# Kernel tuning notes

Hardware: AMD Instinct MI355X
Metric: run time of the kernel (lower is better)

The kernel has to match this reference:

```python
import jax, jax.numpy as jnp
import numpy as np

B, N, C = 2, 384, 128
D = C // 4          # bottleneck_dim
H = 128             # time_mlp_hidden_dim


def setup_inputs() -> dict:
    key = jax.random.key(0)
    ks = jax.random.split(key, 12)
    s = 0.02
    return {
        "edge_embed": jax.random.normal(ks[0], (B, N, N, C), jnp.float32),
        "edge_mask": jax.random.randint(ks[1], (B, N, N), 0, 2, jnp.int32),
        "r3_t": jax.random.uniform(ks[2], (B,), jnp.float32),
        # linear params stored as [in, out]
        "Wg": jax.random.normal(ks[3], (C, D), jnp.float32) * s,
        "bg": jnp.zeros((D,), jnp.float32),
        "Wv": jax.random.normal(ks[4], (C, D), jnp.float32) * s,
        "bv": jnp.zeros((D,), jnp.float32),
        "Wd": jax.random.normal(ks[5], (C, D), jnp.float32) * s,
        "bd": jnp.zeros((D,), jnp.float32),
        "Wo": jax.random.normal(ks[6], (D, C), jnp.float32) * s,
        "bo": jnp.zeros((C,), jnp.float32),
        "W1": jax.random.normal(ks[7], (1, H), jnp.float32) * s,
        "b1": jnp.zeros((H,), jnp.float32),
        "W2": jax.random.normal(ks[8], (H, 2 * C), jnp.float32) * s,
        "b2": jnp.zeros((2 * C,), jnp.float32),
    }


def reference(edge_embed, edge_mask, r3_t, Wg, bg, Wv, bv, Wd, bd, Wo, bo, W1, b1, W2, b2):
    Bb, Nn, _, Cc = edge_embed.shape
    P = edge_embed.reshape(Bb, Nn * Nn, Cc)          # [B, N^2, C]
    m = (edge_mask.reshape(Bb, Nn * Nn, 1) != 0)
    mf = m.astype(P.dtype)

    fP = P @ Wg + bg                                 # [B, N^2, D]
    gP = P @ Wv + bv                                 # [B, N^2, D]
    fP = jnp.where(m, fP, jnp.asarray(-1e8, P.dtype))
    w = jax.nn.softmax(fP, axis=1)                   # softmax over all edges
    w = w * mf
    w = w / (w.sum(axis=1, keepdims=True) + 1e-8)

    V = jnp.einsum('bnd,bne->bde', w, gP)            # [B, D, D] global context

    hP = jax.nn.softmax(P @ Wd + bd, axis=2)         # softmax over channels
    O = jnp.einsum('bnd,bde->bne', hP, V)            # redistribute
    O = (O @ Wo + bo).reshape(Bb, Nn, Nn, Cc)

    # FiLM conditioned on timestep (torch GELU is exact erf form)
    t = r3_t.reshape(Bb, 1)
    t_emb = jax.nn.gelu(t @ W1 + b1, approximate=False) @ W2 + b2
    scale, shift = jnp.split(t_emb, 2, axis=-1)
    O = O * (1 + scale[:, None, None, :]) + shift[:, None, None, :]

    return edge_embed + O
```

## Files before the change

### kernel.cpp

```cpp
#include <hip/hip_runtime.h>
#include <hip/hip_bf16.h>
#include <math.h>

#define N2 147456
#define CC 128
#define TILES 2304

#define WS_VACC 0
#define WS_S    2048
#define WS_FS   2112
#define WS_SH   2368

typedef __attribute__((ext_vector_type(8))) __bf16 bf16x8;
typedef __attribute__((ext_vector_type(4))) __bf16 bf16x4;
typedef __attribute__((ext_vector_type(4))) float f32x4;

#define MFMA16(a_, b_, c_) __builtin_amdgcn_mfma_f32_16x16x32_bf16((a_), (b_), (c_), 0, 0, 0)

__global__ __launch_bounds__(256) void k0_init(
    const float* __restrict__ r3t,
    const float* __restrict__ W1, const float* __restrict__ b1,
    const float* __restrict__ W2, const float* __restrict__ b2,
    float* __restrict__ ws)
{
    const int t = threadIdx.x, bx = blockIdx.x;
    if (bx > 0) {
        const int i = (bx - 1) * 256 + t;
        if (i < 2112) ws[i] = 0.0f;
        return;
    }
    __shared__ float h[2][128];
    {
        const int b = t >> 7, j = t & 127;
        const float x = r3t[b] * W1[j] + b1[j];
        h[b][j] = 0.5f * x * (1.0f + erff(x * 0.7071067811865475f));
    }
    __syncthreads();
    const int j2 = t;
    float acc0 = b2[j2], acc1 = b2[j2];
    for (int k = 0; k < 128; ++k) {
        const float w2 = W2[k * 256 + j2];
        acc0 += h[0][k] * w2;
        acc1 += h[1][k] * w2;
    }
    if (j2 < 128) {
        ws[WS_FS + j2]       = 1.0f + acc0;
        ws[WS_FS + 128 + j2] = 1.0f + acc1;
    } else {
        ws[WS_SH + (j2 - 128)]       = acc0;
        ws[WS_SH + 128 + (j2 - 128)] = acc1;
    }
}

__global__ __launch_bounds__(256, 3) void k1_accum(
    const float* __restrict__ P, const int* __restrict__ mask,
    const float* __restrict__ Wg, const float* __restrict__ bg,
    const float* __restrict__ Wv, const float* __restrict__ bv,
    float* __restrict__ ws)
{
    __shared__ __bf16 ef_t[32][72];
    __shared__ __bf16 gv_t[32][72];

    const int t  = threadIdx.x;
    const int b  = blockIdx.y;
    const int w  = t >> 6;
    const int l  = t & 63;
    const int lr = l & 15;
    const int lg = l >> 4;

    bf16x8 wfrag[2][2][4];
    #pragma unroll
    for (int nt = 0; nt < 2; ++nt)
      #pragma unroll
      for (int ks = 0; ks < 4; ++ks) {
        const int base = (ks * 32 + 8 * lg) * 32 + nt * 16 + lr;
        bf16x8 f0, f1;
        #pragma unroll
        for (int i = 0; i < 8; ++i) {
            f0[i] = (__bf16)Wg[base + i * 32];
            f1[i] = (__bf16)Wv[base + i * 32];
        }
        wfrag[0][nt][ks] = f0;
        wfrag[1][nt][ks] = f1;
      }
    const float bgv[2] = { bg[lr], bg[lr + 16] };
    const float bvv[2] = { bv[lr], bv[lr + 16] };

    const int mt = w >> 1, ntq = w & 1;
    f32x4 vacc = {0.f, 0.f, 0.f, 0.f};
    float accS = 0.f;
    const int sd = t >> 3, ss = t & 7;

    const float* Pb = P + (size_t)b * N2 * CC;
    const int*   mb = mask + (size_t)b * N2;

    for (int tile = blockIdx.x; tile < TILES; tile += gridDim.x) {
        const int row0 = tile * 64 + w * 16;
        const float* prow = Pb + (size_t)(row0 + lr) * CC + 8 * lg;

        bf16x8 afrag[4];
        #pragma unroll
        for (int ks = 0; ks < 4; ++ks) {
            const float4 a0 = *(const float4*)(prow + ks * 32);
            const float4 a1 = *(const float4*)(prow + ks * 32 + 4);
            bf16x8 f;
            f[0] = (__bf16)a0.x; f[1] = (__bf16)a0.y; f[2] = (__bf16)a0.z; f[3] = (__bf16)a0.w;
            f[4] = (__bf16)a1.x; f[5] = (__bf16)a1.y; f[6] = (__bf16)a1.z; f[7] = (__bf16)a1.w;
            afrag[ks] = f;
        }

        f32x4 facc0 = {0,0,0,0}, facc1 = {0,0,0,0}, gacc0 = {0,0,0,0}, gacc1 = {0,0,0,0};
        #pragma unroll
        for (int ks = 0; ks < 4; ++ks) {
            facc0 = MFMA16(afrag[ks], wfrag[0][0][ks], facc0);
            facc1 = MFMA16(afrag[ks], wfrag[0][1][ks], facc1);
            gacc0 = MFMA16(afrag[ks], wfrag[1][0][ks], gacc0);
            gacc1 = MFMA16(afrag[ks], wfrag[1][1][ks], gacc1);
        }

        const int4 mk4 = *(const int4*)&mb[row0 + lg * 4];
        const int mk[4] = { mk4.x, mk4.y, mk4.z, mk4.w };

        bf16x4 pe0, pe1, pg0, pg1;
        #pragma unroll
        for (int r = 0; r < 4; ++r) {
            pe0[r] = (__bf16)(mk[r] ? __expf(facc0[r] + bgv[0]) : 0.0f);
            pe1[r] = (__bf16)(mk[r] ? __expf(facc1[r] + bgv[1]) : 0.0f);
            pg0[r] = (__bf16)(gacc0[r] + bvv[0]);
            pg1[r] = (__bf16)(gacc1[r] + bvv[1]);
        }
        const int cbase = w * 16 + lg * 4;
        *(bf16x4*)&ef_t[lr     ][cbase] = pe0;
        *(bf16x4*)&ef_t[lr + 16][cbase] = pe1;
        *(bf16x4*)&gv_t[lr     ][cbase] = pg0;
        *(bf16x4*)&gv_t[lr + 16][cbase] = pg1;
        __syncthreads();

        #pragma unroll
        for (int ks = 0; ks < 2; ++ks) {
            const bf16x8 ea = *(const bf16x8*)&ef_t[mt  * 16 + lr][ks * 32 + 8 * lg];
            const bf16x8 gb = *(const bf16x8*)&gv_t[ntq * 16 + lr][ks * 32 + 8 * lg];
            vacc = MFMA16(ea, gb, vacc);
        }
        {
            const bf16x8 ev = *(const bf16x8*)&ef_t[sd][ss * 8];
            float s = 0.f;
            #pragma unroll
            for (int i = 0; i < 8; ++i) s += (float)ev[i];
            accS += s;
        }
        __syncthreads();
    }

    #pragma unroll
    for (int r = 0; r < 4; ++r) {
        const int d = mt * 16 + lg * 4 + r;
        const int e = ntq * 16 + lr;
        atomicAdd(ws + WS_VACC + b * 1024 + d * 32 + e, vacc[r]);
    }
    accS += __shfl_xor(accS, 1);
    accS += __shfl_xor(accS, 2);
    accS += __shfl_xor(accS, 4);
    if (ss == 0) atomicAdd(ws + WS_S + b * 32 + sd, accS);
}

__global__ __launch_bounds__(256, 3) void k3_out(
    const float* __restrict__ P,
    const float* __restrict__ Wd, const float* __restrict__ bd,
    const float* __restrict__ Wo, const float* __restrict__ bo,
    const float* __restrict__ ws, float* __restrict__ out)
{
    __shared__ float  u_lds[32][132];
    __shared__ __bf16 h_t[64][40];
    __shared__ float  fin_V[1024];
    __shared__ float  fin_fs[128];
    __shared__ float  fin_b2[128];

    const int t  = threadIdx.x;
    const int b  = blockIdx.y;
    const int w  = t >> 6, l = t & 63, lr = l & 15, lg = l >> 4;

    if (t < 128) {
        const float fs = ws[WS_FS + b * 128 + t];
        fin_fs[t] = fs;
        fin_b2[t] = bo[t] * fs + ws[WS_SH + b * 128 + t];
    }
    #pragma unroll
    for (int i = 0; i < 4; ++i) {
        const int idx = t + i * 256;
        const int d = idx >> 5;
        const float s = ws[WS_S + b * 32 + d];
        fin_V[idx] = ws[WS_VACC + b * 1024 + idx] / (s * (1.0f + 1e-8f));
    }

    bf16x8 wdfrag[2][4];
    #pragma unroll
    for (int nt = 0; nt < 2; ++nt)
      #pragma unroll
      for (int ks = 0; ks < 4; ++ks) {
        const int base = (ks * 32 + 8 * lg) * 32 + nt * 16 + lr;
        bf16x8 f;
        #pragma unroll
        for (int i = 0; i < 8; ++i) f[i] = (__bf16)Wd[base + i * 32];
        wdfrag[nt][ks] = f;
      }
    float bdv[8];
    #pragma unroll
    for (int r = 0; r < 4; ++r) {
        bdv[r]     = bd[lg * 4 + r];
        bdv[4 + r] = bd[16 + lg * 4 + r];
    }

    __syncthreads();

    #pragma unroll
    for (int i = 0; i < 16; ++i) {
        const int idx = t + i * 256;
        const int d = idx >> 7, c = idx & 127;
        float acc = 0.0f;
        #pragma unroll
        for (int e = 0; e < 32; ++e) acc += fin_V[d * 32 + e] * Wo[e * 128 + c];
        u_lds[d][c] = acc * fin_fs[c];
    }
    __syncthreads();

    bf16x8 ufrag[8];
    #pragma unroll
    for (int nt = 0; nt < 8; ++nt) {
        bf16x8 f;
        #pragma unroll
        for (int i = 0; i < 8; ++i) f[i] = (__bf16)u_lds[8 * lg + i][nt * 16 + lr];
        ufrag[nt] = f;
    }
    float b2v[8][4];
    #pragma unroll
    for (int nt = 0; nt < 8; ++nt) {
        const float4 v = *(const float4*)&fin_b2[nt * 16 + lg * 4];
        b2v[nt][0] = v.x; b2v[nt][1] = v.y; b2v[nt][2] = v.z; b2v[nt][3] = v.w;
    }

    const float* Pb = P + (size_t)b * N2 * CC;
    float*       Ob = out + (size_t)b * N2 * CC;

    for (int tile = TILES - 1 - blockIdx.x; tile >= 0; tile -= gridDim.x) {
        const int row0 = tile * 64 + w * 16;
        const float* prow = Pb + (size_t)(row0 + lr) * CC + 8 * lg;

        bf16x8 afrag[4];
        #pragma unroll
        for (int ks = 0; ks < 4; ++ks) {
            const float4 a0 = *(const float4*)(prow + ks * 32);
            const float4 a1 = *(const float4*)(prow + ks * 32 + 4);
            bf16x8 f;
            f[0] = (__bf16)a0.x; f[1] = (__bf16)a0.y; f[2] = (__bf16)a0.z; f[3] = (__bf16)a0.w;
            f[4] = (__bf16)a1.x; f[5] = (__bf16)a1.y; f[6] = (__bf16)a1.z; f[7] = (__bf16)a1.w;
            afrag[ks] = f;
        }

        f32x4 dacc0 = {0,0,0,0}, dacc1 = {0,0,0,0};
        #pragma unroll
        for (int ks = 0; ks < 4; ++ks) {
            dacc0 = MFMA16(wdfrag[0][ks], afrag[ks], dacc0);
            dacc1 = MFMA16(wdfrag[1][ks], afrag[ks], dacc1);
        }

        float v[8];
        #pragma unroll
        for (int r = 0; r < 4; ++r) {
            v[r]     = dacc0[r] + bdv[r];
            v[4 + r] = dacc1[r] + bdv[4 + r];
        }
        float m = v[0];
        #pragma unroll
        for (int j = 1; j < 8; ++j) m = fmaxf(m, v[j]);
        m = fmaxf(m, __shfl_xor(m, 16));
        m = fmaxf(m, __shfl_xor(m, 32));
        float e[8], s = 0.f;
        #pragma unroll
        for (int j = 0; j < 8; ++j) { e[j] = __expf(v[j] - m); s += e[j]; }
        s += __shfl_xor(s, 16);
        s += __shfl_xor(s, 32);
        const float inv = 1.0f / s;

        bf16x4 h0, h1;
        #pragma unroll
        for (int r = 0; r < 4; ++r) {
            h0[r] = (__bf16)(e[r] * inv);
            h1[r] = (__bf16)(e[4 + r] * inv);
        }
        const int hrow = w * 16 + lr;
        *(bf16x4*)&h_t[hrow][lg * 4]      = h0;
        *(bf16x4*)&h_t[hrow][16 + lg * 4] = h1;
        const bf16x8 hf = *(const bf16x8*)&h_t[hrow][8 * lg];

        #pragma unroll
        for (int nt = 0; nt < 8; ++nt) {
            f32x4 ci;
            ci[0] = b2v[nt][0]; ci[1] = b2v[nt][1]; ci[2] = b2v[nt][2]; ci[3] = b2v[nt][3];
            const f32x4 oacc = MFMA16(ufrag[nt], hf, ci);
            const size_t off = (size_t)(row0 + lr) * CC + nt * 16 + lg * 4;
            const float4 p4 = *(const float4*)(Pb + off);
            float4 o4;
            o4.x = p4.x + oacc[0]; o4.y = p4.y + oacc[1];
            o4.z = p4.z + oacc[2]; o4.w = p4.w + oacc[3];
            *(float4*)(Ob + off) = o4;
        }
    }
}

extern "C" void kernel_launch(void* const* d_in, const int* in_sizes, int n_in,
                              void* d_out, int out_size, void* d_ws, size_t ws_size,
                              hipStream_t stream) {
    const float* P   = (const float*)d_in[0];
    const int*   msk = (const int*)d_in[1];
    const float* r3t = (const float*)d_in[2];
    const float* Wg  = (const float*)d_in[3];
    const float* bg  = (const float*)d_in[4];
    const float* Wv  = (const float*)d_in[5];
    const float* bv  = (const float*)d_in[6];
    const float* Wd  = (const float*)d_in[7];
    const float* bd  = (const float*)d_in[8];
    const float* Wo  = (const float*)d_in[9];
    const float* bo  = (const float*)d_in[10];
    const float* W1  = (const float*)d_in[11];
    const float* b1  = (const float*)d_in[12];
    const float* W2  = (const float*)d_in[13];
    const float* b2  = (const float*)d_in[14];
    float* ws  = (float*)d_ws;
    float* out = (float*)d_out;

    hipLaunchKernelGGL(k0_init,  dim3(10),      dim3(256), 0, stream, r3t, W1, b1, W2, b2, ws);
    hipLaunchKernelGGL(k1_accum, dim3(384, 2),  dim3(256), 0, stream, P, msk, Wg, bg, Wv, bv, ws);
    hipLaunchKernelGGL(k3_out,   dim3(768, 2),  dim3(256), 0, stream, P, Wd, bd, Wo, bo, ws, out);
}
```

Before: 133.8 us.

## Hoist V·Wo prologue into a separate kernel and prefetch residual loads

The per-block prologue of the output kernel, which normalised V, multiplied it by Wo and repacked the result into bf16 MFMA fragments, moves into a new two-block mid kernel. That kernel writes the packed fragments and the fused bias/shift vector to the workspace. The output kernel now loads those fragments directly, drops its large LDS buffers, and raises its launch bound to 4 blocks per SM. The residual P loads for the epilogue are also issued at the start of each tile alongside the A-fragment loads, which adds register pressure, and the extra kernel launch adds a small serial cost.

```diff
diff --git a/kernel.cpp b/kernel.cpp
--- a/kernel.cpp
+++ b/kernel.cpp
@@ -6,10 +6,12 @@
 #define CC 128
 #define TILES 2304
 
-#define WS_VACC 0
-#define WS_S    2048
-#define WS_FS   2112
-#define WS_SH   2368
+#define WS_VACC  0
+#define WS_S     2048
+#define WS_FS    2112
+#define WS_SH    2368
+#define WS_UPACK 2624
+#define WS_B2P   6720
 
 typedef __attribute__((ext_vector_type(8))) __bf16 bf16x8;
 typedef __attribute__((ext_vector_type(4))) __bf16 bf16x4;
@@ -164,35 +166,73 @@
     if (ss == 0) atomicAdd(ws + WS_S + b * 32 + sd, accS);
 }
 
-__global__ __launch_bounds__(256, 3) void k3_out(
-    const float* __restrict__ P,
-    const float* __restrict__ Wd, const float* __restrict__ bd,
+__global__ __launch_bounds__(256) void k2_mid(
     const float* __restrict__ Wo, const float* __restrict__ bo,
-    const float* __restrict__ ws, float* __restrict__ out)
+    float* __restrict__ ws)
 {
-    __shared__ float  u_lds[32][132];
-    __shared__ __bf16 h_t[64][40];
-    __shared__ float  fin_V[1024];
-    __shared__ float  fin_fs[128];
-    __shared__ float  fin_b2[128];
-
-    const int t  = threadIdx.x;
-    const int b  = blockIdx.y;
-    const int w  = t >> 6, l = t & 63, lr = l & 15, lg = l >> 4;
-
-    if (t < 128) {
-        const float fs = ws[WS_FS + b * 128 + t];
-        fin_fs[t] = fs;
-        fin_b2[t] = bo[t] * fs + ws[WS_SH + b * 128 + t];
-    }
+    __shared__ float V[1024];
+    __shared__ float wo[32][128];
+    __shared__ float fs[128];
+    const int t = threadIdx.x, b = blockIdx.x;
+
+    if (t < 128) fs[t] = ws[WS_FS + b * 128 + t];
     #pragma unroll
     for (int i = 0; i < 4; ++i) {
         const int idx = t + i * 256;
         const int d = idx >> 5;
         const float s = ws[WS_S + b * 32 + d];
-        fin_V[idx] = ws[WS_VACC + b * 1024 + idx] / (s * (1.0f + 1e-8f));
-    }
-
+        V[idx] = ws[WS_VACC + b * 1024 + idx] / (s * (1.0f + 1e-8f));
+    }
+    #pragma unroll
+    for (int i = 0; i < 4; ++i) {
+        const int j = t + i * 256;
+        ((float4*)&wo[0][0])[j] = ((const float4*)Wo)[j];
+    }
+    __syncthreads();
+
+    const int c = t & 127, dh = t >> 7;
+    float wcol[32];
+    #pragma unroll
+    for (int e = 0; e < 32; ++e) wcol[e] = wo[e][c];
+    const float fsc = fs[c];
+    if (dh == 0) ws[WS_B2P + b * 128 + c] = bo[c] * fsc + ws[WS_SH + b * 128 + c];
+
+    __bf16* dst = (__bf16*)(ws + WS_UPACK);
+    #pragma unroll
+    for (int dd = 0; dd < 16; ++dd) {
+        const int d = dh * 16 + dd;
+        float acc = 0.0f;
+        #pragma unroll
+        for (int e = 0; e < 32; ++e) acc += V[d * 32 + e] * wcol[e];
+        acc *= fsc;
+        const int lg = d >> 3, ii = d & 7, nt = c >> 4, lr = c & 15;
+        dst[(((size_t)b * 8 + nt) * 64 + (lg * 16 + lr)) * 8 + ii] = (__bf16)acc;
+    }
+}
+
+__global__ __launch_bounds__(256, 4) void k3_out(
+    const float* __restrict__ P,
+    const float* __restrict__ Wd, const float* __restrict__ bd,
+    const float* __restrict__ ws, float* __restrict__ out)
+{
+    __shared__ __bf16 h_t[64][40];
+
+    const int t  = threadIdx.x;
+    const int b  = blockIdx.y;
+    const int w  = t >> 6, l = t & 63, lr = l & 15, lg = l >> 4;
+
+    bf16x8 ufrag[8];
+    {
+        const bf16x8* up = (const bf16x8*)(ws + WS_UPACK) + (size_t)b * 512 + l;
+        #pragma unroll
+        for (int nt = 0; nt < 8; ++nt) ufrag[nt] = up[nt * 64];
+    }
+    float b2v[8][4];
+    #pragma unroll
+    for (int nt = 0; nt < 8; ++nt) {
+        const float4 v = *(const float4*)(ws + WS_B2P + b * 128 + nt * 16 + lg * 4);
+        b2v[nt][0] = v.x; b2v[nt][1] = v.y; b2v[nt][2] = v.z; b2v[nt][3] = v.w;
+    }
     bf16x8 wdfrag[2][4];
     #pragma unroll
     for (int nt = 0; nt < 2; ++nt)
@@ -211,46 +251,29 @@
         bdv[4 + r] = bd[16 + lg * 4 + r];
     }
 
-    __syncthreads();
-
-    #pragma unroll
-    for (int i = 0; i < 16; ++i) {
-        const int idx = t + i * 256;
-        const int d = idx >> 7, c = idx & 127;
-        float acc = 0.0f;
-        #pragma unroll
-        for (int e = 0; e < 32; ++e) acc += fin_V[d * 32 + e] * Wo[e * 128 + c];
-        u_lds[d][c] = acc * fin_fs[c];
-    }
-    __syncthreads();
-
-    bf16x8 ufrag[8];
-    #pragma unroll
-    for (int nt = 0; nt < 8; ++nt) {
-        bf16x8 f;
-        #pragma unroll
-        for (int i = 0; i < 8; ++i) f[i] = (__bf16)u_lds[8 * lg + i][nt * 16 + lr];
-        ufrag[nt] = f;
-    }
-    float b2v[8][4];
-    #pragma unroll
-    for (int nt = 0; nt < 8; ++nt) {
-        const float4 v = *(const float4*)&fin_b2[nt * 16 + lg * 4];
-        b2v[nt][0] = v.x; b2v[nt][1] = v.y; b2v[nt][2] = v.z; b2v[nt][3] = v.w;
-    }
-
     const float* Pb = P + (size_t)b * N2 * CC;
     float*       Ob = out + (size_t)b * N2 * CC;
 
     for (int tile = TILES - 1 - blockIdx.x; tile >= 0; tile -= gridDim.x) {
         const int row0 = tile * 64 + w * 16;
-        const float* prow = Pb + (size_t)(row0 + lr) * CC + 8 * lg;
+        const size_t rbase = (size_t)(row0 + lr) * CC;
+        const float* prow = Pb + rbase + 8 * lg;
+
+        float4 a4[8];
+        #pragma unroll
+        for (int ks = 0; ks < 4; ++ks) {
+            a4[2 * ks]     = *(const float4*)(prow + ks * 32);
+            a4[2 * ks + 1] = *(const float4*)(prow + ks * 32 + 4);
+        }
+        float4 p4v[8];
+        #pragma unroll
+        for (int nt = 0; nt < 8; ++nt)
+            p4v[nt] = *(const float4*)(Pb + rbase + nt * 16 + lg * 4);
 
         bf16x8 afrag[4];
         #pragma unroll
         for (int ks = 0; ks < 4; ++ks) {
-            const float4 a0 = *(const float4*)(prow + ks * 32);
-            const float4 a1 = *(const float4*)(prow + ks * 32 + 4);
+            const float4 a0 = a4[2 * ks], a1 = a4[2 * ks + 1];
             bf16x8 f;
             f[0] = (__bf16)a0.x; f[1] = (__bf16)a0.y; f[2] = (__bf16)a0.z; f[3] = (__bf16)a0.w;
             f[4] = (__bf16)a1.x; f[5] = (__bf16)a1.y; f[6] = (__bf16)a1.z; f[7] = (__bf16)a1.w;
@@ -298,12 +321,10 @@
             f32x4 ci;
             ci[0] = b2v[nt][0]; ci[1] = b2v[nt][1]; ci[2] = b2v[nt][2]; ci[3] = b2v[nt][3];
             const f32x4 oacc = MFMA16(ufrag[nt], hf, ci);
-            const size_t off = (size_t)(row0 + lr) * CC + nt * 16 + lg * 4;
-            const float4 p4 = *(const float4*)(Pb + off);
             float4 o4;
-            o4.x = p4.x + oacc[0]; o4.y = p4.y + oacc[1];
-            o4.z = p4.z + oacc[2]; o4.w = p4.w + oacc[3];
-            *(float4*)(Ob + off) = o4;
+            o4.x = p4v[nt].x + oacc[0]; o4.y = p4v[nt].y + oacc[1];
+            o4.z = p4v[nt].z + oacc[2]; o4.w = p4v[nt].w + oacc[3];
+            *(float4*)(Ob + rbase + nt * 16 + lg * 4) = o4;
         }
     }
 }
@@ -331,5 +352,6 @@
 
     hipLaunchKernelGGL(k0_init,  dim3(10),      dim3(256), 0, stream, r3t, W1, b1, W2, b2, ws);
     hipLaunchKernelGGL(k1_accum, dim3(384, 2),  dim3(256), 0, stream, P, msk, Wg, bg, Wv, bv, ws);
-    hipLaunchKernelGGL(k3_out,   dim3(768, 2),  dim3(256), 0, stream, P, Wd, bd, Wo, bo, ws, out);
-}
+    hipLaunchKernelGGL(k2_mid,   dim3(2),       dim3(256), 0, stream, Wo, bo, ws);
+    hipLaunchKernelGGL(k3_out,   dim3(768, 2),  dim3(256), 0, stream, P, Wd, bd, ws, out);
+}
```

After: 174.3 us. +30.3%, slower.
